# Kernel tuning notes

Measured on AMD Instinct MI355X. Metric: run time of the kernel, lower is better.

Reference implementation:

```python
import jax, jax.numpy as jnp
import numpy as np

H = 1024   # hidden_size
IN = 512   # input_size
B = 256    # batch
T = 256    # timesteps

DT = 0.1
DELTA_T = 1.0
Z_MIN = 0.001
Z_MAX = 0.1


def setup_inputs() -> dict:
    key = jax.random.key(0)
    ks = jax.random.split(key, 10)
    bound = 1.0 / np.sqrt(H)
    u = lambda k, shape: jax.random.uniform(k, shape, jnp.float32, -bound, bound)
    return {
        "x":   jax.random.normal(ks[0], (T, IN, B), jnp.float32),
        "c_x": u(ks[1], (H, 1)),
        "c_u": u(ks[2], (H, 1)),
        "c_U": u(ks[3], (H, 1)),
        "w_r": u(ks[4], (H, H)),
        "p_r": u(ks[5], (H, IN)),
        "b_r": u(ks[6], (H, 1)),
        "g_z": u(ks[7], (H, 1)),
        "K":   u(ks[8], (H, H)),
        "p_z": u(ks[9], (H, IN)),
    }


def reference(x, c_x, c_u, c_U, w_r, p_r, b_r, g_z, K, p_z):
    # Gate-rate constants (computed once; they don't depend on state)
    z_x = Z_MIN + (Z_MAX - Z_MIN) * jax.nn.sigmoid(c_x)   # (H,1)
    z_u = Z_MIN + (Z_MAX - Z_MIN) * jax.nn.sigmoid(c_u)   # (H,1)
    Ucap = 0.9 * jax.nn.sigmoid(c_U)                      # (H,1)
    Ucap_sg = jax.lax.stop_gradient(Ucap)                 # clamp bound is detached in torch

    def step(carry, xt):
        X, U, v = carry                   # each (H,B); xt: (IN,B)
        r = jax.nn.sigmoid(v)             # r_t from previous v_t
        X_new = z_x + (1.0 - z_x) * X - DELTA_T * U * X * r
        U_new = Ucap * z_u + (1.0 - z_u) * U + DELTA_T * Ucap * (1.0 - U) * r
        U_new = jnp.clip(U_new, Ucap_sg, 1.0)
        z_t = DT * jax.nn.sigmoid(K @ r + p_z @ xt + g_z)
        v_new = (1.0 - z_t) * v + DT * (w_r @ (U_new * X_new * r) + p_r @ xt + b_r)
        return (X_new, U_new, v_new), v_new

    X0 = jnp.ones((H, B), jnp.float32)
    U0 = jnp.full((H, B), 0.9, jnp.float32)
    v0 = jnp.zeros((H, B), jnp.float32)

    (_, _, _), vs = jax.lax.scan(step, (X0, U0, v0), x)
    # return hidden-state trajectory as (T, batch, hidden)
    return jnp.transpose(vs, (0, 2, 1))
```

## Files before the change

### kernel.cpp

```cpp
#include <hip/hip_runtime.h>
#include <hip/hip_bf16.h>

#define Hh 1024
#define INs 512
#define Bb 256
#define Tt 256
#define DT_ 0.1f
#define Z_MIN_ 0.001f
#define Z_MAX_ 0.1f
#define KW (Hh + INs)
#define NB 256

typedef __attribute__((ext_vector_type(8))) short short8;
typedef __attribute__((ext_vector_type(4))) float f32x4;

__device__ __forceinline__ float sigmoidf_(float x) {
    return 1.0f / (1.0f + __expf(-x));
}

__device__ __forceinline__ unsigned short f2bf(float f) {
    union { float f; unsigned u; } v; v.f = f;
    unsigned r = v.u + 0x7FFFu + ((v.u >> 16) & 1u);
    return (unsigned short)(r >> 16);
}

__global__ __launch_bounds__(256) void build_weights(
    const float* __restrict__ Km, const float* __restrict__ p_z,
    const float* __restrict__ w_r, const float* __restrict__ p_r,
    unsigned short* __restrict__ W1, unsigned short* __restrict__ W2) {
    int idx = blockIdx.x * 256 + threadIdx.x;
    int h = idx / KW, k = idx % KW;
    float a = (k < Hh) ? Km[h * Hh + k] : p_z[h * INs + (k - Hh)];
    float b = (k < Hh) ? w_r[h * Hh + k] : p_r[h * INs + (k - Hh)];
    W1[idx] = f2bf(a);
    W2[idx] = f2bf(b);
}

__global__ __launch_bounds__(256) void transpose_x(
    const float* __restrict__ x, unsigned short* __restrict__ xT) {
    __shared__ unsigned short tile[64][65];
    int t = blockIdx.z;
    int i0 = blockIdx.y * 64;
    int b0 = blockIdx.x * 64;
    int c = threadIdx.x & 63, rbase = threadIdx.x >> 6;
    const float* xp = x + (size_t)t * INs * Bb;
#pragma unroll
    for (int r = 0; r < 16; ++r) {
        int row = r * 4 + rbase;
        tile[row][c] = f2bf(xp[(size_t)(i0 + row) * Bb + (b0 + c)]);
    }
    __syncthreads();
    unsigned short* op = xT + (size_t)t * Bb * INs;
#pragma unroll
    for (int r = 0; r < 16; ++r) {
        int brow = r * 4 + rbase;
        op[(size_t)(b0 + brow) * INs + (i0 + c)] = tile[c][brow];
    }
}

__global__ __launch_bounds__(256) void precomp_gates(
    const float* __restrict__ c_x, const float* __restrict__ c_u,
    const float* __restrict__ c_U,
    float* __restrict__ zxv, float* __restrict__ zuv, float* __restrict__ Ucv) {
    int h = blockIdx.x * 256 + threadIdx.x;
    zxv[h] = Z_MIN_ + (Z_MAX_ - Z_MIN_) * sigmoidf_(c_x[h]);
    zuv[h] = Z_MIN_ + (Z_MAX_ - Z_MIN_) * sigmoidf_(c_u[h]);
    Ucv[h] = 0.9f * sigmoidf_(c_U[h]);
}

__global__ __launch_bounds__(256) void init_state(
    const float* __restrict__ zxv, const float* __restrict__ zuv,
    const float* __restrict__ Ucv,
    unsigned short* __restrict__ R0, unsigned short* __restrict__ M0,
    unsigned* __restrict__ bar) {
    int idx = blockIdx.x * 256 + threadIdx.x;
    if (idx < 8) bar[idx * 32] = 0;
    int h = idx & (Hh - 1);
    float zx = zxv[h], zu = zuv[h], Uc = Ucv[h];
    const float r = 0.5f;
    float Xn = zx + (1.0f - zx) - 0.45f;
    float Un = Uc * zu + (1.0f - zu) * 0.9f + Uc * 0.05f;
    Un = fminf(fmaxf(Un, Uc), 1.0f);
    R0[idx] = f2bf(r);
    M0[idx] = f2bf(Un * Xn * r);
}

__global__ __launch_bounds__(256, 1) void persist_kernel(
    const unsigned short* __restrict__ W1, const unsigned short* __restrict__ W2,
    const unsigned short* __restrict__ xT,
    unsigned short* __restrict__ Rb0, unsigned short* __restrict__ Rb1,
    unsigned short* __restrict__ Mb0, unsigned short* __restrict__ Mb1,
    float* __restrict__ out,
    const float* __restrict__ g_z, const float* __restrict__ b_r,
    const float* __restrict__ zxv, const float* __restrict__ zuv,
    const float* __restrict__ Ucv, unsigned* __restrict__ bar) {

    const int tid = threadIdx.x;
    const int wave = tid >> 6, lane = tid & 63;
    const int m = lane & 15, q = lane >> 4;
    const int kq = wave;
    const int rowg = blockIdx.x >> 3;
    const int colg = blockIdx.x & 7;

    unsigned* cnt = bar + (unsigned)colg * 32;

    const int krec = kq * 256;
    const int kx = kq * 128;
    const int bcol0 = colg * 32 + m;
    const int bcol1 = bcol0 + 16;

    short8 wf1[2][12], wf2[2][12];
#pragma unroll
    for (int rs = 0; rs < 2; ++rs) {
        const int arow = rowg * 32 + rs * 16 + m;
        const unsigned short* w1r = W1 + (size_t)arow * KW + krec + q * 8;
        const unsigned short* w2r = W2 + (size_t)arow * KW + krec + q * 8;
#pragma unroll
        for (int c = 0; c < 8; ++c) {
            wf1[rs][c] = *(const short8*)(w1r + c * 32);
            wf2[rs][c] = *(const short8*)(w2r + c * 32);
        }
        const unsigned short* w1x = W1 + (size_t)arow * KW + Hh + kx + q * 8;
        const unsigned short* w2x = W2 + (size_t)arow * KW + Hh + kx + q * 8;
#pragma unroll
        for (int c = 0; c < 4; ++c) {
            wf1[rs][8 + c] = *(const short8*)(w1x + c * 32);
            wf2[rs][8 + c] = *(const short8*)(w2x + c * 32);
        }
    }

    const int rs_e = wave >> 1, ch_e = wave & 1;
    const int h04 = rowg * 32 + rs_e * 16 + q * 4;
    const int bcol_e = colg * 32 + ch_e * 16 + m;
    const int a1 = rs_e * 4 + ch_e * 2;

    f32x4 zx4 = *(const f32x4*)(zxv + h04);
    f32x4 zu4 = *(const f32x4*)(zuv + h04);
    f32x4 Uc4 = *(const f32x4*)(Ucv + h04);
    f32x4 gz4 = *(const f32x4*)(g_z + h04);
    f32x4 br4 = *(const f32x4*)(b_r + h04);

    f32x4 vr, Xr, Ur;
#pragma unroll
    for (int e = 0; e < 4; ++e) {
        vr[e] = 0.0f;
        float Xn = zx4[e] + (1.0f - zx4[e]) - 0.45f;
        float Un = Uc4[e] * zu4[e] + (1.0f - zu4[e]) * 0.9f + Uc4[e] * 0.05f;
        Un = fminf(fmaxf(Un, Uc4[e]), 1.0f);
        Xr[e] = Xn; Ur[e] = Un;
    }

    __shared__ f32x4 red[4][8][64];

    short8 xb0[4], xb1[4];
    {
        const unsigned short* xp0 = xT + (size_t)bcol0 * INs + kx + q * 8;
        const unsigned short* xp1 = xT + (size_t)bcol1 * INs + kx + q * 8;
#pragma unroll
        for (int c = 0; c < 4; ++c) {
            xb0[c] = *(const short8*)(xp0 + c * 32);
            xb1[c] = *(const short8*)(xp1 + c * 32);
        }
    }

    for (int t = 0; t < Tt; ++t) {
        const unsigned short* Rt = (t & 1) ? Rb1 : Rb0;
        const unsigned short* Mt = (t & 1) ? Mb1 : Mb0;
        unsigned short* Rn = (t & 1) ? Rb0 : Rb1;
        unsigned short* Mn = (t & 1) ? Mb0 : Mb1;

        f32x4 acc[2][2][2];
#pragma unroll
        for (int rs = 0; rs < 2; ++rs)
#pragma unroll
            for (int ch = 0; ch < 2; ++ch)
#pragma unroll
                for (int mt = 0; mt < 2; ++mt)
                    acc[rs][ch][mt] = (f32x4){0.0f, 0.0f, 0.0f, 0.0f};

#pragma unroll
        for (int c = 0; c < 4; ++c) {
#pragma unroll
            for (int rs = 0; rs < 2; ++rs) {
                acc[rs][0][0] = __builtin_amdgcn_mfma_f32_16x16x32_bf16(wf1[rs][8 + c], xb0[c], acc[rs][0][0], 0, 0, 0);
                acc[rs][1][0] = __builtin_amdgcn_mfma_f32_16x16x32_bf16(wf1[rs][8 + c], xb1[c], acc[rs][1][0], 0, 0, 0);
                acc[rs][0][1] = __builtin_amdgcn_mfma_f32_16x16x32_bf16(wf2[rs][8 + c], xb0[c], acc[rs][0][1], 0, 0, 0);
                acc[rs][1][1] = __builtin_amdgcn_mfma_f32_16x16x32_bf16(wf2[rs][8 + c], xb1[c], acc[rs][1][1], 0, 0, 0);
            }
        }

        if (t + 1 < Tt) {
            const unsigned short* xn0 = xT + (size_t)(t + 1) * Bb * INs
                                      + (size_t)bcol0 * INs + kx + q * 8;
            const unsigned short* xn1 = xT + (size_t)(t + 1) * Bb * INs
                                      + (size_t)bcol1 * INs + kx + q * 8;
#pragma unroll
            for (int c = 0; c < 4; ++c) {
                xb0[c] = *(const short8*)(xn0 + c * 32);
                xb1[c] = *(const short8*)(xn1 + c * 32);
            }
        }

        const unsigned short* rp0 = Rt + (size_t)bcol0 * Hh + krec + q * 8;
        const unsigned short* rp1 = Rt + (size_t)bcol1 * Hh + krec + q * 8;
        const unsigned short* mp0 = Mt + (size_t)bcol0 * Hh + krec + q * 8;
        const unsigned short* mp1 = Mt + (size_t)bcol1 * Hh + krec + q * 8;

#pragma unroll
        for (int c = 0; c < 8; ++c) {
            short8 bR0 = *(const short8*)(rp0 + c * 32);
            short8 bR1 = *(const short8*)(rp1 + c * 32);
            short8 bM0 = *(const short8*)(mp0 + c * 32);
            short8 bM1 = *(const short8*)(mp1 + c * 32);
#pragma unroll
            for (int rs = 0; rs < 2; ++rs) {
                acc[rs][0][0] = __builtin_amdgcn_mfma_f32_16x16x32_bf16(wf1[rs][c], bR0, acc[rs][0][0], 0, 0, 0);
                acc[rs][1][0] = __builtin_amdgcn_mfma_f32_16x16x32_bf16(wf1[rs][c], bR1, acc[rs][1][0], 0, 0, 0);
                acc[rs][0][1] = __builtin_amdgcn_mfma_f32_16x16x32_bf16(wf2[rs][c], bM0, acc[rs][0][1], 0, 0, 0);
                acc[rs][1][1] = __builtin_amdgcn_mfma_f32_16x16x32_bf16(wf2[rs][c], bM1, acc[rs][1][1], 0, 0, 0);
            }
        }

#pragma unroll
        for (int rs = 0; rs < 2; ++rs)
#pragma unroll
            for (int ch = 0; ch < 2; ++ch)
#pragma unroll
                for (int mt = 0; mt < 2; ++mt)
                    red[kq][rs * 4 + ch * 2 + mt][lane] = acc[rs][ch][mt];
        __syncthreads();

        f32x4 g1 = red[0][a1][lane];
        g1 += red[1][a1][lane];
        g1 += red[2][a1][lane];
        g1 += red[3][a1][lane];
        f32x4 g2 = red[0][a1 + 1][lane];
        g2 += red[1][a1 + 1][lane];
        g2 += red[2][a1 + 1][lane];
        g2 += red[3][a1 + 1][lane];

        {
            f32x4 vv;
            ushort4 rq, mq;
#pragma unroll
            for (int e = 0; e < 4; ++e) {
                float z = DT_ * sigmoidf_(g1[e] + gz4[e]);
                float vnew = (1.0f - z) * vr[e] + DT_ * (g2[e] + br4[e]);
                vr[e] = vnew;
                vv[e] = vnew;
                float r = sigmoidf_(vnew);
                float Xs = Xr[e], Us = Ur[e];
                float Xn = zx4[e] + (1.0f - zx4[e]) * Xs - Us * Xs * r;
                float Un = Uc4[e] * zu4[e] + (1.0f - zu4[e]) * Us
                         + Uc4[e] * (1.0f - Us) * r;
                Un = fminf(fmaxf(Un, Uc4[e]), 1.0f);
                Xr[e] = Xn; Ur[e] = Un;
                unsigned short rb = f2bf(r), mb = f2bf(Un * Xn * r);
                if (e == 0) { rq.x = rb; mq.x = mb; }
                else if (e == 1) { rq.y = rb; mq.y = mb; }
                else if (e == 2) { rq.z = rb; mq.z = mb; }
                else { rq.w = rb; mq.w = mb; }
            }
            const size_t base = (size_t)bcol_e * Hh + h04;
            *(f32x4*)(out + (size_t)t * Bb * Hh + base) = vv;
            *(ushort4*)(Rn + base) = rq;
            *(ushort4*)(Mn + base) = mq;
        }
        __syncthreads();

        if (t + 1 < Tt) {
            if (tid == 0)
                __hip_atomic_fetch_add(cnt, 1u, __ATOMIC_RELAXED,
                                       __HIP_MEMORY_SCOPE_AGENT);
            if (tid == 0) {
                const unsigned tgt = (unsigned)(t + 1) * 32u;
                while (__hip_atomic_load(cnt, __ATOMIC_RELAXED,
                                         __HIP_MEMORY_SCOPE_AGENT) < tgt)
                    __builtin_amdgcn_s_sleep(1);
                asm volatile("buffer_inv sc0" ::: "memory");
            }
            __syncthreads();
        }
    }
}

extern "C" void kernel_launch(void* const* d_in, const int* in_sizes, int n_in,
                              void* d_out, int out_size, void* d_ws, size_t ws_size,
                              hipStream_t stream) {
    const float* x   = (const float*)d_in[0];
    const float* c_x = (const float*)d_in[1];
    const float* c_u = (const float*)d_in[2];
    const float* c_U = (const float*)d_in[3];
    const float* w_r = (const float*)d_in[4];
    const float* p_r = (const float*)d_in[5];
    const float* b_r = (const float*)d_in[6];
    const float* g_z = (const float*)d_in[7];
    const float* Km  = (const float*)d_in[8];
    const float* p_z = (const float*)d_in[9];
    float* out = (float*)d_out;

    char* w = (char*)d_ws;
    unsigned short* W1 = (unsigned short*)w;   w += (size_t)Hh * KW * 2;
    unsigned short* W2 = (unsigned short*)w;   w += (size_t)Hh * KW * 2;
    unsigned short* xT = (unsigned short*)w;   w += (size_t)Tt * Bb * INs * 2;
    unsigned short* Rb0 = (unsigned short*)w;  w += (size_t)Bb * Hh * 2;
    unsigned short* Rb1 = (unsigned short*)w;  w += (size_t)Bb * Hh * 2;
    unsigned short* Mb0 = (unsigned short*)w;  w += (size_t)Bb * Hh * 2;
    unsigned short* Mb1 = (unsigned short*)w;  w += (size_t)Bb * Hh * 2;
    float* zxv = (float*)w;                    w += 4096;
    float* zuv = (float*)w;                    w += 4096;
    float* Ucv = (float*)w;                    w += 4096;
    unsigned* bar = (unsigned*)w;              w += 4096;

    build_weights<<<(Hh * KW) / 256, 256, 0, stream>>>(Km, p_z, w_r, p_r, W1, W2);
    transpose_x<<<dim3(Bb / 64, INs / 64, Tt), 256, 0, stream>>>(x, xT);
    precomp_gates<<<Hh / 256, 256, 0, stream>>>(c_x, c_u, c_U, zxv, zuv, Ucv);
    init_state<<<(Bb * Hh) / 256, 256, 0, stream>>>(zxv, zuv, Ucv, Rb0, Mb0, bar);

    persist_kernel<<<NB, 256, 0, stream>>>(
        W1, W2, xT, Rb0, Rb1, Mb0, Mb1, out,
        g_z, b_r, zxv, zuv, Ucv, bar);
}
```

Before: 2.016 ms.

## Repartition persistent RNN kernel: 8 waves per block, 64-row by 16-column tiles

Blocks now run 512 threads (8 waves), each splitting K eight ways, and the tile shape changes from 32 hidden rows by 32 batch columns to 64 rows by 16 columns. Column groups double to 16, so each barrier group spans 16 blocks instead of 32. Each wave holds fewer weight registers and handles a smaller K slice, which raises latency hiding per CU. The cost is a larger cross-wave LDS reduction over 8 partials, and each lane now does epilogue work on only two hidden elements.

```diff
diff --git a/kernel.cpp b/kernel.cpp
--- a/kernel.cpp
+++ b/kernel.cpp
@@ -13,6 +13,7 @@
 
 typedef __attribute__((ext_vector_type(8))) short short8;
 typedef __attribute__((ext_vector_type(4))) float f32x4;
+typedef __attribute__((ext_vector_type(2))) float f32x2;
 
 __device__ __forceinline__ float sigmoidf_(float x) {
     return 1.0f / (1.0f + __expf(-x));
@@ -74,7 +75,7 @@
     unsigned short* __restrict__ R0, unsigned short* __restrict__ M0,
     unsigned* __restrict__ bar) {
     int idx = blockIdx.x * 256 + threadIdx.x;
-    if (idx < 8) bar[idx * 32] = 0;
+    if (idx < 16) bar[idx * 32] = 0;
     int h = idx & (Hh - 1);
     float zx = zxv[h], zu = zuv[h], Uc = Ucv[h];
     const float r = 0.5f;
@@ -85,7 +86,7 @@
     M0[idx] = f2bf(Un * Xn * r);
 }
 
-__global__ __launch_bounds__(256, 1) void persist_kernel(
+__global__ __launch_bounds__(512, 1) void persist_kernel(
     const unsigned short* __restrict__ W1, const unsigned short* __restrict__ W2,
     const unsigned short* __restrict__ xT,
     unsigned short* __restrict__ Rb0, unsigned short* __restrict__ Rb1,
@@ -99,68 +100,63 @@
     const int wave = tid >> 6, lane = tid & 63;
     const int m = lane & 15, q = lane >> 4;
     const int kq = wave;
-    const int rowg = blockIdx.x >> 3;
-    const int colg = blockIdx.x & 7;
+    const int rowg = blockIdx.x >> 4;
+    const int colg = blockIdx.x & 15;
 
     unsigned* cnt = bar + (unsigned)colg * 32;
 
-    const int krec = kq * 256;
-    const int kx = kq * 128;
-    const int bcol0 = colg * 32 + m;
-    const int bcol1 = bcol0 + 16;
-
-    short8 wf1[2][12], wf2[2][12];
-#pragma unroll
-    for (int rs = 0; rs < 2; ++rs) {
-        const int arow = rowg * 32 + rs * 16 + m;
+    const int krec = kq * 128;
+    const int kx = kq * 64;
+    const int bcol = colg * 16 + m;
+
+    short8 wf1[4][6], wf2[4][6];
+#pragma unroll
+    for (int rs = 0; rs < 4; ++rs) {
+        const int arow = rowg * 64 + rs * 16 + m;
         const unsigned short* w1r = W1 + (size_t)arow * KW + krec + q * 8;
         const unsigned short* w2r = W2 + (size_t)arow * KW + krec + q * 8;
 #pragma unroll
-        for (int c = 0; c < 8; ++c) {
+        for (int c = 0; c < 4; ++c) {
             wf1[rs][c] = *(const short8*)(w1r + c * 32);
             wf2[rs][c] = *(const short8*)(w2r + c * 32);
         }
         const unsigned short* w1x = W1 + (size_t)arow * KW + Hh + kx + q * 8;
         const unsigned short* w2x = W2 + (size_t)arow * KW + Hh + kx + q * 8;
 #pragma unroll
-        for (int c = 0; c < 4; ++c) {
-            wf1[rs][8 + c] = *(const short8*)(w1x + c * 32);
-            wf2[rs][8 + c] = *(const short8*)(w2x + c * 32);
-        }
-    }
-
-    const int rs_e = wave >> 1, ch_e = wave & 1;
-    const int h04 = rowg * 32 + rs_e * 16 + q * 4;
-    const int bcol_e = colg * 32 + ch_e * 16 + m;
-    const int a1 = rs_e * 4 + ch_e * 2;
-
-    f32x4 zx4 = *(const f32x4*)(zxv + h04);
-    f32x4 zu4 = *(const f32x4*)(zuv + h04);
-    f32x4 Uc4 = *(const f32x4*)(Ucv + h04);
-    f32x4 gz4 = *(const f32x4*)(g_z + h04);
-    f32x4 br4 = *(const f32x4*)(b_r + h04);
-
-    f32x4 vr, Xr, Ur;
-#pragma unroll
-    for (int e = 0; e < 4; ++e) {
-        vr[e] = 0.0f;
-        float Xn = zx4[e] + (1.0f - zx4[e]) - 0.45f;
-        float Un = Uc4[e] * zu4[e] + (1.0f - zu4[e]) * 0.9f + Uc4[e] * 0.05f;
-        Un = fminf(fmaxf(Un, Uc4[e]), 1.0f);
-        Xr[e] = Xn; Ur[e] = Un;
-    }
-
-    __shared__ f32x4 red[4][8][64];
-
-    short8 xb0[4], xb1[4];
+        for (int c = 0; c < 2; ++c) {
+            wf1[rs][4 + c] = *(const short8*)(w1x + c * 32);
+            wf2[rs][4 + c] = *(const short8*)(w2x + c * 32);
+        }
+    }
+
+    const int rs_e = wave >> 1, eh = wave & 1;
+    const int h2 = rowg * 64 + rs_e * 16 + q * 4 + eh * 2;
+    const int bcol_e = colg * 16 + m;
+
+    f32x2 zx2 = *(const f32x2*)(zxv + h2);
+    f32x2 zu2 = *(const f32x2*)(zuv + h2);
+    f32x2 Uc2 = *(const f32x2*)(Ucv + h2);
+    f32x2 gz2 = *(const f32x2*)(g_z + h2);
+    f32x2 br2 = *(const f32x2*)(b_r + h2);
+
+    f32x2 vr, Xr, Ur;
+#pragma unroll
+    for (int j = 0; j < 2; ++j) {
+        vr[j] = 0.0f;
+        float Xn = zx2[j] + (1.0f - zx2[j]) - 0.45f;
+        float Un = Uc2[j] * zu2[j] + (1.0f - zu2[j]) * 0.9f + Uc2[j] * 0.05f;
+        Un = fminf(fmaxf(Un, Uc2[j]), 1.0f);
+        Xr[j] = Xn; Ur[j] = Un;
+    }
+
+    __shared__ f32x4 red[8][4][2][64];
+
+    short8 xb[2];
     {
-        const unsigned short* xp0 = xT + (size_t)bcol0 * INs + kx + q * 8;
-        const unsigned short* xp1 = xT + (size_t)bcol1 * INs + kx + q * 8;
-#pragma unroll
-        for (int c = 0; c < 4; ++c) {
-            xb0[c] = *(const short8*)(xp0 + c * 32);
-            xb1[c] = *(const short8*)(xp1 + c * 32);
-        }
+        const unsigned short* xp = xT + (size_t)bcol * INs + kx + q * 8;
+#pragma unroll
+        for (int c = 0; c < 2; ++c)
+            xb[c] = *(const short8*)(xp + c * 32);
     }
 
     for (int t = 0; t < Tt; ++t) {
@@ -169,102 +165,83 @@
         unsigned short* Rn = (t & 1) ? Rb0 : Rb1;
         unsigned short* Mn = (t & 1) ? Mb0 : Mb1;
 
-        f32x4 acc[2][2][2];
-#pragma unroll
-        for (int rs = 0; rs < 2; ++rs)
-#pragma unroll
-            for (int ch = 0; ch < 2; ++ch)
-#pragma unroll
-                for (int mt = 0; mt < 2; ++mt)
-                    acc[rs][ch][mt] = (f32x4){0.0f, 0.0f, 0.0f, 0.0f};
+        f32x4 acc[4][2];
+#pragma unroll
+        for (int rs = 0; rs < 4; ++rs)
+#pragma unroll
+            for (int mt = 0; mt < 2; ++mt)
+                acc[rs][mt] = (f32x4){0.0f, 0.0f, 0.0f, 0.0f};
+
+#pragma unroll
+        for (int c = 0; c < 2; ++c)
+#pragma unroll
+            for (int rs = 0; rs < 4; ++rs) {
+                acc[rs][0] = __builtin_amdgcn_mfma_f32_16x16x32_bf16(wf1[rs][4 + c], xb[c], acc[rs][0], 0, 0, 0);
+                acc[rs][1] = __builtin_amdgcn_mfma_f32_16x16x32_bf16(wf2[rs][4 + c], xb[c], acc[rs][1], 0, 0, 0);
+            }
+
+        if (t + 1 < Tt) {
+            const unsigned short* xn = xT + (size_t)(t + 1) * Bb * INs
+                                     + (size_t)bcol * INs + kx + q * 8;
+#pragma unroll
+            for (int c = 0; c < 2; ++c)
+                xb[c] = *(const short8*)(xn + c * 32);
+        }
+
+        const unsigned short* rp = Rt + (size_t)bcol * Hh + krec + q * 8;
+        const unsigned short* mp = Mt + (size_t)bcol * Hh + krec + q * 8;
 
 #pragma unroll
         for (int c = 0; c < 4; ++c) {
-#pragma unroll
-            for (int rs = 0; rs < 2; ++rs) {
-                acc[rs][0][0] = __builtin_amdgcn_mfma_f32_16x16x32_bf16(wf1[rs][8 + c], xb0[c], acc[rs][0][0], 0, 0, 0);
-                acc[rs][1][0] = __builtin_amdgcn_mfma_f32_16x16x32_bf16(wf1[rs][8 + c], xb1[c], acc[rs][1][0], 0, 0, 0);
-                acc[rs][0][1] = __builtin_amdgcn_mfma_f32_16x16x32_bf16(wf2[rs][8 + c], xb0[c], acc[rs][0][1], 0, 0, 0);
-                acc[rs][1][1] = __builtin_amdgcn_mfma_f32_16x16x32_bf16(wf2[rs][8 + c], xb1[c], acc[rs][1][1], 0, 0, 0);
-            }
-        }
-
-        if (t + 1 < Tt) {
-            const unsigned short* xn0 = xT + (size_t)(t + 1) * Bb * INs
-                                      + (size_t)bcol0 * INs + kx + q * 8;
-            const unsigned short* xn1 = xT + (size_t)(t + 1) * Bb * INs
-                                      + (size_t)bcol1 * INs + kx + q * 8;
-#pragma unroll
-            for (int c = 0; c < 4; ++c) {
-                xb0[c] = *(const short8*)(xn0 + c * 32);
-                xb1[c] = *(const short8*)(xn1 + c * 32);
-            }
-        }
-
-        const unsigned short* rp0 = Rt + (size_t)bcol0 * Hh + krec + q * 8;
-        const unsigned short* rp1 = Rt + (size_t)bcol1 * Hh + krec + q * 8;
-        const unsigned short* mp0 = Mt + (size_t)bcol0 * Hh + krec + q * 8;
-        const unsigned short* mp1 = Mt + (size_t)bcol1 * Hh + krec + q * 8;
-
-#pragma unroll
-        for (int c = 0; c < 8; ++c) {
-            short8 bR0 = *(const short8*)(rp0 + c * 32);
-            short8 bR1 = *(const short8*)(rp1 + c * 32);
-            short8 bM0 = *(const short8*)(mp0 + c * 32);
-            short8 bM1 = *(const short8*)(mp1 + c * 32);
-#pragma unroll
-            for (int rs = 0; rs < 2; ++rs) {
-                acc[rs][0][0] = __builtin_amdgcn_mfma_f32_16x16x32_bf16(wf1[rs][c], bR0, acc[rs][0][0], 0, 0, 0);
-                acc[rs][1][0] = __builtin_amdgcn_mfma_f32_16x16x32_bf16(wf1[rs][c], bR1, acc[rs][1][0], 0, 0, 0);
-                acc[rs][0][1] = __builtin_amdgcn_mfma_f32_16x16x32_bf16(wf2[rs][c], bM0, acc[rs][0][1], 0, 0, 0);
-                acc[rs][1][1] = __builtin_amdgcn_mfma_f32_16x16x32_bf16(wf2[rs][c], bM1, acc[rs][1][1], 0, 0, 0);
-            }
-        }
-
-#pragma unroll
-        for (int rs = 0; rs < 2; ++rs)
-#pragma unroll
-            for (int ch = 0; ch < 2; ++ch)
-#pragma unroll
-                for (int mt = 0; mt < 2; ++mt)
-                    red[kq][rs * 4 + ch * 2 + mt][lane] = acc[rs][ch][mt];
+            short8 bR = *(const short8*)(rp + c * 32);
+            short8 bM = *(const short8*)(mp + c * 32);
+#pragma unroll
+            for (int rs = 0; rs < 4; ++rs) {
+                acc[rs][0] = __builtin_amdgcn_mfma_f32_16x16x32_bf16(wf1[rs][c], bR, acc[rs][0], 0, 0, 0);
+                acc[rs][1] = __builtin_amdgcn_mfma_f32_16x16x32_bf16(wf2[rs][c], bM, acc[rs][1], 0, 0, 0);
+            }
+        }
+
+#pragma unroll
+        for (int rs = 0; rs < 4; ++rs)
+#pragma unroll
+            for (int mt = 0; mt < 2; ++mt)
+                red[kq][rs][mt][lane] = acc[rs][mt];
         __syncthreads();
 
-        f32x4 g1 = red[0][a1][lane];
-        g1 += red[1][a1][lane];
-        g1 += red[2][a1][lane];
-        g1 += red[3][a1][lane];
-        f32x4 g2 = red[0][a1 + 1][lane];
-        g2 += red[1][a1 + 1][lane];
-        g2 += red[2][a1 + 1][lane];
-        g2 += red[3][a1 + 1][lane];
-
         {
-            f32x4 vv;
-            ushort4 rq, mq;
-#pragma unroll
-            for (int e = 0; e < 4; ++e) {
-                float z = DT_ * sigmoidf_(g1[e] + gz4[e]);
-                float vnew = (1.0f - z) * vr[e] + DT_ * (g2[e] + br4[e]);
-                vr[e] = vnew;
-                vv[e] = vnew;
+            f32x2 g1 = {0.0f, 0.0f}, g2 = {0.0f, 0.0f};
+#pragma unroll
+            for (int k2 = 0; k2 < 8; ++k2) {
+                const float* p1 = (const float*)&red[k2][rs_e][0][lane];
+                const float* p2 = (const float*)&red[k2][rs_e][1][lane];
+                g1 += *(const f32x2*)(p1 + eh * 2);
+                g2 += *(const f32x2*)(p2 + eh * 2);
+            }
+
+            f32x2 vv;
+            ushort2 rq, mq;
+#pragma unroll
+            for (int j = 0; j < 2; ++j) {
+                float z = DT_ * sigmoidf_(g1[j] + gz2[j]);
+                float vnew = (1.0f - z) * vr[j] + DT_ * (g2[j] + br2[j]);
+                vr[j] = vnew;
+                vv[j] = vnew;
                 float r = sigmoidf_(vnew);
-                float Xs = Xr[e], Us = Ur[e];
-                float Xn = zx4[e] + (1.0f - zx4[e]) * Xs - Us * Xs * r;
-                float Un = Uc4[e] * zu4[e] + (1.0f - zu4[e]) * Us
-                         + Uc4[e] * (1.0f - Us) * r;
-                Un = fminf(fmaxf(Un, Uc4[e]), 1.0f);
-                Xr[e] = Xn; Ur[e] = Un;
+                float Xs = Xr[j], Us = Ur[j];
+                float Xn = zx2[j] + (1.0f - zx2[j]) * Xs - Us * Xs * r;
+                float Un = Uc2[j] * zu2[j] + (1.0f - zu2[j]) * Us
+                         + Uc2[j] * (1.0f - Us) * r;
+                Un = fminf(fmaxf(Un, Uc2[j]), 1.0f);
+                Xr[j] = Xn; Ur[j] = Un;
                 unsigned short rb = f2bf(r), mb = f2bf(Un * Xn * r);
-                if (e == 0) { rq.x = rb; mq.x = mb; }
-                else if (e == 1) { rq.y = rb; mq.y = mb; }
-                else if (e == 2) { rq.z = rb; mq.z = mb; }
-                else { rq.w = rb; mq.w = mb; }
-            }
-            const size_t base = (size_t)bcol_e * Hh + h04;
-            *(f32x4*)(out + (size_t)t * Bb * Hh + base) = vv;
-            *(ushort4*)(Rn + base) = rq;
-            *(ushort4*)(Mn + base) = mq;
+                if (j == 0) { rq.x = rb; mq.x = mb; }
+                else        { rq.y = rb; mq.y = mb; }
+            }
+            const size_t base = (size_t)bcol_e * Hh + h2;
+            *(f32x2*)(out + (size_t)t * Bb * Hh + base) = vv;
+            *(ushort2*)(Rn + base) = rq;
+            *(ushort2*)(Mn + base) = mq;
         }
         __syncthreads();
 
@@ -273,7 +250,7 @@
                 __hip_atomic_fetch_add(cnt, 1u, __ATOMIC_RELAXED,
                                        __HIP_MEMORY_SCOPE_AGENT);
             if (tid == 0) {
-                const unsigned tgt = (unsigned)(t + 1) * 32u;
+                const unsigned tgt = (unsigned)(t + 1) * 16u;
                 while (__hip_atomic_load(cnt, __ATOMIC_RELAXED,
                                          __HIP_MEMORY_SCOPE_AGENT) < tgt)
                     __builtin_amdgcn_s_sleep(1);
@@ -317,7 +294,7 @@
     precomp_gates<<<Hh / 256, 256, 0, stream>>>(c_x, c_u, c_U, zxv, zuv, Ucv);
     init_state<<<(Bb * Hh) / 256, 256, 0, stream>>>(zxv, zuv, Ucv, Rb0, Mb0, bar);
 
-    persist_kernel<<<NB, 256, 0, stream>>>(
+    persist_kernel<<<NB, 512, 0, stream>>>(
         W1, W2, xT, Rb0, Rb1, Mb0, Mb1, out,
         g_z, b_r, zxv, zuv, Ucv, bar);
 }
```

After: 1.884 ms. -6.5%, faster.
